# Kernel optimization log

Hardware: AMD Instinct MI355X
Metric: run time of the kernel (lower is better)

The kernel has to match this reference:

```python
import jax, jax.numpy as jnp
import numpy as np

B, S, DIM, N, D = 1, 2688, 1536, 12, 128
C = D // 2  # 64 complex pairs per head
EPS = 1e-06


def rms_norm(x, g, eps=EPS):
    # x: [B, S, DIM] -- norm over full model dim, as in WanRMSNorm
    xf = x.astype(jnp.float32)
    return (xf * jax.lax.rsqrt(jnp.mean(xf * xf, axis=-1, keepdims=True) + eps)) * g


def rope_apply(x, f, h, w, freqs_c):
    # x: [B, S, N, D]; freqs_c: complex64 [1024, C]; f*h*w == S (full-seq case)
    s1 = C - 2 * (C // 3)  # 22 (temporal)
    s2 = C // 3            # 21 (height), 21 (width)
    ff = freqs_c[:f, :s1]
    fh = freqs_c[:h, s1:s1 + s2]
    fw = freqs_c[:w, s1 + s2:]
    fi = jnp.concatenate([
        jnp.broadcast_to(ff[:, None, None, :], (f, h, w, s1)),
        jnp.broadcast_to(fh[None, :, None, :], (f, h, w, s2)),
        jnp.broadcast_to(fw[None, None, :, :], (f, h, w, s2)),
    ], axis=-1).reshape(f * h * w, 1, C)  # [S, 1, C]
    xr = x.astype(jnp.float32).reshape(B, S, N, C, 2)
    xc = jax.lax.complex(xr[..., 0], xr[..., 1])          # [B, S, N, C]
    out = xc * fi[None]                                    # broadcast over B, N
    return jnp.stack([out.real, out.imag], axis=-1).reshape(B, S, N, D)


def setup_inputs() -> dict:
    key = jax.random.key(0)
    ks = jax.random.split(key, 12)
    w_scale = 0.02
    # deterministic rope angles (faithful structure: exp(i*theta) per axis slice)
    pos = np.arange(1024, dtype=np.float32)
    inv = 1.0 / (10000.0 ** (np.arange(C, dtype=np.float32) / C))
    ang = pos[:, None] * inv[None, :]
    return {
        "x": jax.random.normal(ks[0], (B, S, DIM), jnp.float32),
        "seq_lens": jnp.full((B,), S, dtype=jnp.int32),
        "grid_sizes": jnp.array([[6, 16, 28]], dtype=jnp.int32),
        "freqs_cos": jnp.asarray(np.cos(ang), jnp.float32),
        "freqs_sin": jnp.asarray(np.sin(ang), jnp.float32),
        "Wq": jax.random.normal(ks[1], (DIM, DIM), jnp.float32) * w_scale,
        "bq": jnp.zeros((DIM,), jnp.float32),
        "Wk": jax.random.normal(ks[2], (DIM, DIM), jnp.float32) * w_scale,
        "bk": jnp.zeros((DIM,), jnp.float32),
        "Wv": jax.random.normal(ks[3], (DIM, DIM), jnp.float32) * w_scale,
        "bv": jnp.zeros((DIM,), jnp.float32),
        "Wo": jax.random.normal(ks[4], (DIM, DIM), jnp.float32) * w_scale,
        "bo": jnp.zeros((DIM,), jnp.float32),
        "gq": jnp.ones((DIM,), jnp.float32),
        "gk": jnp.ones((DIM,), jnp.float32),
    }


def reference(x, seq_lens, grid_sizes, freqs_cos, freqs_sin,
              Wq, bq, Wk, bk, Wv, bv, Wo, bo, gq, gk):
    f, h, w = (int(grid_sizes[0, 0]), int(grid_sizes[0, 1]), int(grid_sizes[0, 2]))
    freqs_c = jax.lax.complex(freqs_cos, freqs_sin)  # [1024, C]

    q = rms_norm(x @ Wq.T + bq, gq).reshape(B, S, N, D)
    k = rms_norm(x @ Wk.T + bk, gk).reshape(B, S, N, D)
    v = (x @ Wv.T + bv).reshape(B, S, N, D)

    q = rope_apply(q, f, h, w, freqs_c)
    k = rope_apply(k, f, h, w, freqs_c)

    # SDPA with key-length masking (k_lens)
    scale = 1.0 / jnp.sqrt(jnp.float32(D))
    scores = jnp.einsum("bqnd,bknd->bnqk", q, k) * scale  # [B, N, S, S]
    kmask = jnp.arange(S)[None, :] < seq_lens[:, None]     # [B, S]
    scores = jnp.where(kmask[:, None, None, :], scores, -jnp.inf)
    attn = jax.nn.softmax(scores, axis=-1)
    out = jnp.einsum("bnqk,bknd->bqnd", attn, v).reshape(B, S, DIM)
    return out @ Wo.T + bo
```

## Files before the change

### kernel.cpp

```cpp
#include <hip/hip_runtime.h>
#include <hip/hip_bf16.h>
#include <stdint.h>

#define S_LEN 2688
#define DIM   1536
#define NH    12
#define HD    128
#define QKV_N 4608

typedef __attribute__((ext_vector_type(8)))  short bf16x8;
typedef __attribute__((ext_vector_type(4)))  float f32x4;
typedef __attribute__((ext_vector_type(16))) float f32x16;

__device__ inline ushort f2bf(float f) {
    uint32_t u = __float_as_uint(f);
    uint32_t r = (u + 0x7fffu + ((u >> 16) & 1u)) >> 16;
    return (ushort)r;
}
__device__ inline float bf2f(uint u) { return __uint_as_float(u << 16); }
__device__ inline float fexp2(float x) {
    float r;
    asm("v_exp_f32 %0, %1" : "=v"(r) : "v"(x));
    return r;
}
__device__ inline uint cvtpk(float lo, float hi) {
    uint r;
    asm("v_cvt_pk_bf16_f32 %0, %1, %2" : "=v"(r) : "v"(lo), "v"(hi));
    return r;
}

#define GLOAD16(gp, lp) __builtin_amdgcn_global_load_lds( \
    (__attribute__((address_space(1))) const void*)(gp),  \
    (__attribute__((address_space(3))) void*)(lp), 16, 0, 0)

__global__ __launch_bounds__(256) void convert_all(
    const float* __restrict__ x,
    const float* __restrict__ wq, const float* __restrict__ wk,
    const float* __restrict__ wv, const float* __restrict__ wo,
    ushort* __restrict__ xb, ushort* __restrict__ wb)
{
    const size_t NX4 = (size_t)S_LEN * DIM / 4;
    const size_t NW4 = (size_t)DIM * DIM / 4;
    size_t i = (size_t)blockIdx.x * 256 + threadIdx.x;
    const float* src; ushort* dst;
    if (i < NX4)            { src = x;  dst = xb; }
    else if (i < NX4+1*NW4) { src = wq; dst = wb;                        i -= NX4; }
    else if (i < NX4+2*NW4) { src = wk; dst = wb + 1*(size_t)DIM*DIM;    i -= NX4+1*NW4; }
    else if (i < NX4+3*NW4) { src = wv; dst = wb + 2*(size_t)DIM*DIM;    i -= NX4+2*NW4; }
    else if (i < NX4+4*NW4) { src = wo; dst = wb + 3*(size_t)DIM*DIM;    i -= NX4+3*NW4; }
    else return;
    float4 v = reinterpret_cast<const float4*>(src)[i];
    ushort4 o = { f2bf(v.x), f2bf(v.y), f2bf(v.z), f2bf(v.w) };
    reinterpret_cast<ushort4*>(dst)[i] = o;
}

__global__ __launch_bounds__(256) void gemm_qkv(
    const ushort* __restrict__ A, const ushort* __restrict__ B,
    const float* __restrict__ bq, const float* __restrict__ bk,
    const float* __restrict__ bv,
    ushort* __restrict__ qkb, ushort* __restrict__ v_t, int K)
{
    __shared__ ushort At[128 * 64];
    __shared__ ushort Bt[128 * 64];
    const int tid  = threadIdx.x;
    const int wave = tid >> 6, lane = tid & 63;
    const int lid  = blockIdx.y * 21 + blockIdx.x;
    const int xcd  = lid & 7, pos = lid >> 3;
    const int wgid = (xcd < 4 ? xcd * 95 : 4 * 95 + (xcd - 4) * 94) + pos;
    const int m0 = (wgid % 21) * 128, n0 = (wgid / 21) * 128;
    const int wr = wave >> 1, wc = wave & 1;
    const int r = lane & 15, g = lane >> 4;
    const int srow = wave * 8 + (lane >> 3);
    const int scol = (lane & 7) * 8;

    f32x4 acc[4][4] = {};

    for (int k0 = 0; k0 < K; k0 += 64) {
        const ushort* Ag = A + (size_t)m0 * K + k0;
        const ushort* Bg = B + (size_t)n0 * K + k0;
#pragma unroll
        for (int t = 0; t < 4; ++t) {
            GLOAD16(Ag + (size_t)(t*32 + srow) * K + scol, &At[t*2048 + wave*512]);
            GLOAD16(Bg + (size_t)(t*32 + srow) * K + scol, &Bt[t*2048 + wave*512]);
        }
        asm volatile("s_waitcnt vmcnt(0)" ::: "memory");
        __syncthreads();
#pragma unroll
        for (int kk = 0; kk < 2; ++kk) {
            bf16x8 af[4], bfr[4];
#pragma unroll
            for (int i = 0; i < 4; ++i)
                af[i] = *reinterpret_cast<const bf16x8*>(
                    &At[(wr*64 + i*16 + r) * 64 + kk*32 + g*8]);
#pragma unroll
            for (int i = 0; i < 4; ++i)
                bfr[i] = *reinterpret_cast<const bf16x8*>(
                    &Bt[(wc*64 + i*16 + r) * 64 + kk*32 + g*8]);
#pragma unroll
            for (int mi = 0; mi < 4; ++mi)
#pragma unroll
                for (int ni = 0; ni < 4; ++ni)
                    acc[mi][ni] = __builtin_amdgcn_mfma_f32_16x16x32_bf16(
                        af[mi], bfr[ni], acc[mi][ni], 0, 0, 0);
        }
        __syncthreads();
    }

    if (n0 < 2*DIM) {
#pragma unroll
        for (int ni = 0; ni < 4; ++ni) {
            int col = n0 + wc*64 + ni*16 + r;
            float bias = (col < DIM) ? bq[col] : bk[col - DIM];
#pragma unroll
            for (int mi = 0; mi < 4; ++mi) {
                int row = m0 + wr*64 + mi*16 + g*4;
#pragma unroll
                for (int j = 0; j < 4; ++j)
                    qkb[(size_t)(row + j) * (2*DIM) + col] =
                        f2bf(acc[mi][ni][j] + bias);
            }
        }
    } else {
#pragma unroll
        for (int ni = 0; ni < 4; ++ni) {
            int d = n0 - 2*DIM + wc*64 + ni*16 + r;
            float bias = bv[d];
#pragma unroll
            for (int mi = 0; mi < 4; ++mi) {
                int row = m0 + wr*64 + mi*16 + g*4;
                uint2 pkt;
                pkt.x = cvtpk(acc[mi][ni][0] + bias, acc[mi][ni][1] + bias);
                pkt.y = cvtpk(acc[mi][ni][2] + bias, acc[mi][ni][3] + bias);
                *reinterpret_cast<uint2*>(&v_t[(size_t)d * S_LEN + row]) = pkt;
            }
        }
    }
}

__global__ __launch_bounds__(256) void gemm_bt2(
    const ushort* __restrict__ A, const ushort* __restrict__ B,
    const float* __restrict__ b0,
    float* __restrict__ C, int M, int N, int K)
{
    __shared__ ushort At[128 * 64];
    __shared__ ushort Bt[64 * 64];
    const int tid  = threadIdx.x;
    const int wave = tid >> 6, lane = tid & 63;
    const int m0 = blockIdx.x * 128, n0 = blockIdx.y * 64;
    const int wr = wave >> 1, wc = wave & 1;
    const int r = lane & 15, g = lane >> 4;
    const int srow = wave * 8 + (lane >> 3);
    const int scol = (lane & 7) * 8;
    const int brow[2] = { (0*256+tid)>>3, (1*256+tid)>>3 };
    const int bcol = (tid & 7) * 8;

    f32x4 acc[4][2] = {};

    for (int k0 = 0; k0 < K; k0 += 64) {
        const ushort* Ag = A + (size_t)m0 * K + k0;
        const ushort* Bg = B + (size_t)n0 * K + k0;
#pragma unroll
        for (int t = 0; t < 4; ++t)
            GLOAD16(Ag + (size_t)(t*32 + srow) * K + scol, &At[t*2048 + wave*512]);
#pragma unroll
        for (int t = 0; t < 2; ++t)
            GLOAD16(Bg + (size_t)brow[t] * K + bcol, &Bt[(t*256 + wave*64) * 8]);
        asm volatile("s_waitcnt vmcnt(0)" ::: "memory");
        __syncthreads();
#pragma unroll
        for (int kk = 0; kk < 2; ++kk) {
            bf16x8 af[4], bfr[2];
#pragma unroll
            for (int i = 0; i < 4; ++i)
                af[i] = *reinterpret_cast<const bf16x8*>(
                    &At[(wr*64 + i*16 + r) * 64 + kk*32 + g*8]);
#pragma unroll
            for (int i = 0; i < 2; ++i)
                bfr[i] = *reinterpret_cast<const bf16x8*>(
                    &Bt[(wc*32 + i*16 + r) * 64 + kk*32 + g*8]);
#pragma unroll
            for (int mi = 0; mi < 4; ++mi)
#pragma unroll
                for (int ni = 0; ni < 2; ++ni)
                    acc[mi][ni] = __builtin_amdgcn_mfma_f32_16x16x32_bf16(
                        af[mi], bfr[ni], acc[mi][ni], 0, 0, 0);
        }
        __syncthreads();
    }

#pragma unroll
    for (int ni = 0; ni < 2; ++ni) {
        int col = n0 + wc*32 + ni*16 + r;
        float bias = b0[col];
#pragma unroll
        for (int mi = 0; mi < 4; ++mi) {
            int row = m0 + wr*64 + mi*16 + g*4;
#pragma unroll
            for (int j = 0; j < 4; ++j)
                C[(size_t)(row + j) * N + col] = acc[mi][ni][j] + bias;
        }
    }
}

__global__ __launch_bounds__(256) void normrope(
    const ushort* __restrict__ qkb, const int* __restrict__ gsz,
    const float* __restrict__ gq, const float* __restrict__ gk,
    const float* __restrict__ fcos, const float* __restrict__ fsin,
    ushort* __restrict__ q_r, ushort* __restrict__ k_r)
{
    const int s   = blockIdx.x;
    const int tid = threadIdx.x;
    const int wave = tid >> 6, lane = tid & 63;
    const uint* qrow = reinterpret_cast<const uint*>(qkb + (size_t)s * (2*DIM));
    const uint* krow = qrow + DIM/2;

    float2 qv[3], kv[3];
    float sq = 0.f, sk = 0.f;
#pragma unroll
    for (int i = 0; i < 3; ++i) {
        int p = tid + i*256;
        uint uq = qrow[p], uk = krow[p];
        qv[i].x = bf2f(uq & 0xffffu); qv[i].y = bf2f(uq >> 16);
        kv[i].x = bf2f(uk & 0xffffu); kv[i].y = bf2f(uk >> 16);
        sq += qv[i].x*qv[i].x + qv[i].y*qv[i].y;
        sk += kv[i].x*kv[i].x + kv[i].y*kv[i].y;
    }
#pragma unroll
    for (int off = 1; off < 64; off <<= 1) {
        sq += __shfl_xor(sq, off);
        sk += __shfl_xor(sk, off);
    }
    __shared__ float red[4][2];
    if (lane == 0) { red[wave][0] = sq; red[wave][1] = sk; }
    __syncthreads();
    sq = red[0][0] + red[1][0] + red[2][0] + red[3][0];
    sk = red[0][1] + red[1][1] + red[2][1] + red[3][1];
    const float rmsq = rsqrtf(sq * (1.f/DIM) + 1e-6f);
    const float rmsk = rsqrtf(sk * (1.f/DIM) + 1e-6f);

    const int hh = gsz[1], ww = gsz[2];
    const int fidx = s / (hh*ww), rem = s % (hh*ww);
    const int hidx = rem / ww,  widx = rem % ww;
    const float qscale = rmsq * (0.08838834764831845f * 1.4426950408889634f);

#pragma unroll
    for (int i = 0; i < 3; ++i) {
        int p = tid + i*256;
        int c = p & 63, head = p >> 6;
        int coord = (c < 22) ? fidx : (c < 43) ? hidx : widx;
        float cv = fcos[coord*64 + c], sv = fsin[coord*64 + c];
        float2 gqv = reinterpret_cast<const float2*>(gq)[p];
        float2 gkv = reinterpret_cast<const float2*>(gk)[p];
        float a = qv[i].x * qscale * gqv.x, b = qv[i].y * qscale * gqv.y;
        uint qo = cvtpk(a*cv - b*sv, a*sv + b*cv);
        a = kv[i].x * rmsk * gkv.x; b = kv[i].y * rmsk * gkv.y;
        uint ko = cvtpk(a*cv - b*sv, a*sv + b*cv);
        size_t off = (((size_t)head * S_LEN + s) * HD + 2*c) >> 1;
        reinterpret_cast<uint*>(q_r)[off] = qo;
        reinterpret_cast<uint*>(k_r)[off] = ko;
    }
}

__global__ __launch_bounds__(256) void attn_fwd(
    const ushort* __restrict__ q_r, const ushort* __restrict__ k_r,
    const ushort* __restrict__ v_t, const int* __restrict__ seq_lens,
    ushort* __restrict__ attn_out)
{
    __shared__ ushort Kl[2][64 * 128];
    __shared__ ushort Vl[2][128 * 64];
    const int tid  = threadIdx.x;
    const int wave = tid >> 6, lane = tid & 63;
    const int n  = blockIdx.y;
    const int seq = seq_lens[0];
    const int khalf = wave & 1, pair = wave >> 1;
    const int ql = lane & 31, h = lane >> 5, sw = lane & 7;
    const int qrow = blockIdx.x * 64 + pair * 32 + ql;
    const ushort* Qh = q_r + (size_t)n * S_LEN * HD;
    const ushort* Kh = k_r + (size_t)n * S_LEN * HD;
    const ushort* Vh = v_t + (size_t)n * HD * S_LEN;

    const int kj_row[4] = { (0*256+tid)>>4, (1*256+tid)>>4, (2*256+tid)>>4, (3*256+tid)>>4 };
    const int kj_w  = tid & 15;
    const int vj_d[4]  = { (0*256+tid)>>3, (1*256+tid)>>3, (2*256+tid)>>3, (3*256+tid)>>3 };
    const int vj_w  = tid & 7;

    bf16x8 qf[8];
#pragma unroll
    for (int c = 0; c < 8; ++c)
        qf[c] = *reinterpret_cast<const bf16x8*>(Qh + (size_t)qrow * HD + c*16 + h*8);

    f32x16 oacc[4] = {};
    float mrun = -1e30f, lrun = 0.f;

    const int nt = (seq + 63) >> 6;

#define STAGE(buf, kbase)                                                     \
    do {                                                                      \
        _Pragma("unroll")                                                     \
        for (int t = 0; t < 4; ++t) {                                         \
            int row = kj_row[t];                                              \
            GLOAD16(Kh + (size_t)((kbase) + row) * HD + ((kj_w ^ (row & 7)) * 8), \
                    &Kl[buf][(t*256 + wave*64) * 8]);                         \
        }                                                                     \
        _Pragma("unroll")                                                     \
        for (int t = 0; t < 4; ++t) {                                         \
            int d = vj_d[t];                                                  \
            GLOAD16(Vh + (size_t)d * S_LEN + (kbase) + ((vj_w ^ (d & 7)) * 8), \
                    &Vl[buf][(t*256 + wave*64) * 8]);                         \
        }                                                                     \
    } while (0)

    STAGE(0, 0);
    asm volatile("s_waitcnt vmcnt(0)" ::: "memory");
    __syncthreads();

    int cur = 0;
    for (int kt = 0; kt < nt; ++kt) {
        const int k0 = kt * 64 + khalf * 32;
        if (kt + 1 < nt) STAGE(cur ^ 1, (kt+1) * 64);

        f32x16 sf = {};
        const ushort* kl = &Kl[cur][(khalf*32 + ql) * 128];
#pragma unroll
        for (int c = 0; c < 8; ++c)
            sf = __builtin_amdgcn_mfma_f32_32x32x16_bf16(
                *reinterpret_cast<const bf16x8*>(kl + ((2*c + h) ^ sw) * 8),
                qf[c], sf, 0, 0, 0);
        if (k0 + 32 > seq) {
#pragma unroll
            for (int j = 0; j < 16; ++j)
                if (k0 + (j&3) + 8*(j>>2) + 4*h >= seq) sf[j] = -1e30f;
        }
        float pm = sf[0];
#pragma unroll
        for (int j = 1; j < 16; ++j) pm = fmaxf(pm, sf[j]);
        pm = fmaxf(pm, __shfl_xor(pm, 32));
        if (!__all(pm - mrun <= 8.f)) {
            float mn = fmaxf(mrun, pm);
            float scl = fexp2(mrun - mn);
            mrun = mn;
            lrun *= scl;
#pragma unroll
            for (int db = 0; db < 4; ++db)
#pragma unroll
                for (int j = 0; j < 16; ++j) oacc[db][j] *= scl;
        }
        float ps = 0.f;
#pragma unroll
        for (int j = 0; j < 16; ++j) {
            float e = fexp2(sf[j] - mrun);
            sf[j] = e;
            ps += e;
        }
        ps += __shfl_xor(ps, 32);
        lrun += ps;
        uint u0 = cvtpk(sf[0],  sf[1]),  u1 = cvtpk(sf[2],  sf[3]);
        uint u2 = cvtpk(sf[4],  sf[5]),  u3 = cvtpk(sf[6],  sf[7]);
        uint u4 = cvtpk(sf[8],  sf[9]),  u5 = cvtpk(sf[10], sf[11]);
        uint u6 = cvtpk(sf[12], sf[13]), u7 = cvtpk(sf[14], sf[15]);
        asm("v_permlane32_swap_b32 %0, %1" : "+v"(u0), "+v"(u2));
        asm("v_permlane32_swap_b32 %0, %1" : "+v"(u1), "+v"(u3));
        asm("v_permlane32_swap_b32 %0, %1" : "+v"(u4), "+v"(u6));
        asm("v_permlane32_swap_b32 %0, %1" : "+v"(u5), "+v"(u7));
        union { uint uu[4]; bf16x8 v; } fa, fb;
        fa.uu[0] = u0; fa.uu[1] = u1; fa.uu[2] = u2; fa.uu[3] = u3;
        fb.uu[0] = u4; fb.uu[1] = u5; fb.uu[2] = u6; fb.uu[3] = u7;
#pragma unroll
        for (int db = 0; db < 4; ++db) {
            const ushort* vl = &Vl[cur][(db*32 + ql) * 64];
            oacc[db] = __builtin_amdgcn_mfma_f32_32x32x16_bf16(
                *reinterpret_cast<const bf16x8*>(vl + ((khalf*4 + 0 + h) ^ sw) * 8),
                fa.v, oacc[db], 0, 0, 0);
            oacc[db] = __builtin_amdgcn_mfma_f32_32x32x16_bf16(
                *reinterpret_cast<const bf16x8*>(vl + ((khalf*4 + 2 + h) ^ sw) * 8),
                fb.v, oacc[db], 0, 0, 0);
        }

        if (kt + 1 < nt) {
            asm volatile("s_waitcnt vmcnt(0)" ::: "memory");
            __syncthreads();
            cur ^= 1;
        }
    }
#undef STAGE

    __syncthreads();
    float* Obuf  = (float*)&Kl[0][0];
    float* MLbuf = (float*)&Vl[0][0];
    if (khalf == 1) {
#pragma unroll
        for (int db = 0; db < 4; ++db)
#pragma unroll
            for (int j = 0; j < 16; ++j) {
                int d = db*32 + (j&3) + 8*(j>>2) + 4*h;
                Obuf[pair*4096 + d*32 + ql] = oacc[db][j];
            }
        if (h == 0) { MLbuf[pair*64 + ql] = mrun; MLbuf[pair*64 + 32 + ql] = lrun; }
    }
    __syncthreads();
    if (khalf == 0) {
        float m2 = MLbuf[pair*64 + ql], l2 = MLbuf[pair*64 + 32 + ql];
        float mm = fmaxf(mrun, m2);
        float s1 = fexp2(mrun - mm), s2 = fexp2(m2 - mm);
        float ltot = lrun * s1 + l2 * s2;
        float inv = (ltot > 0.f) ? 1.f / ltot : 0.f;
#pragma unroll
        for (int db = 0; db < 4; ++db)
#pragma unroll
            for (int j = 0; j < 16; ++j) {
                int d = db*32 + (j&3) + 8*(j>>2) + 4*h;
                oacc[db][j] = (oacc[db][j] * s1 +
                               Obuf[pair*4096 + d*32 + ql] * s2) * inv;
            }
#pragma unroll
        for (int db = 0; db < 4; ++db)
#pragma unroll
            for (int jg = 0; jg < 4; ++jg) {
                uint2 pkt;
                pkt.x = cvtpk(oacc[db][jg*4+0], oacc[db][jg*4+1]);
                pkt.y = cvtpk(oacc[db][jg*4+2], oacc[db][jg*4+3]);
                *reinterpret_cast<uint2*>(
                    &attn_out[(size_t)qrow * DIM + n*HD + db*32 + jg*8 + 4*h]) = pkt;
            }
    }
}

extern "C" void kernel_launch(void* const* d_in, const int* in_sizes, int n_in,
                              void* d_out, int out_size, void* d_ws, size_t ws_size,
                              hipStream_t stream)
{
    const float* x    = (const float*)d_in[0];
    const int*   seqL = (const int*)  d_in[1];
    const int*   gsz  = (const int*)  d_in[2];
    const float* fcos = (const float*)d_in[3];
    const float* fsin = (const float*)d_in[4];
    const float* Wq   = (const float*)d_in[5];
    const float* bq   = (const float*)d_in[6];
    const float* Wk   = (const float*)d_in[7];
    const float* bk   = (const float*)d_in[8];
    const float* Wv   = (const float*)d_in[9];
    const float* bv   = (const float*)d_in[10];
    const float* Wo   = (const float*)d_in[11];
    const float* bo   = (const float*)d_in[12];
    const float* gq   = (const float*)d_in[13];
    const float* gk   = (const float*)d_in[14];
    float* out = (float*)d_out;

    char* ws = (char*)d_ws;
    ushort* xb  = (ushort*)ws;
    ushort* wb  = xb  + (size_t)S_LEN * DIM;
    ushort* qkb = wb  + 4*(size_t)DIM*DIM;
    ushort* v_t = qkb + (size_t)S_LEN * 2*DIM;
    ushort* q_r = v_t + (size_t)DIM * S_LEN;
    ushort* k_r = q_r + (size_t)S_LEN * DIM;
    ushort* ao  = k_r + (size_t)S_LEN * DIM;

    convert_all<<<13248, 256, 0, stream>>>(x, Wq, Wk, Wv, Wo, xb, wb);
    gemm_qkv<<<dim3(21, 36), 256, 0, stream>>>(xb, wb, bq, bk, bv,
                                               qkb, v_t, DIM);
    normrope<<<S_LEN, 256, 0, stream>>>(qkb, gsz, gq, gk, fcos, fsin, q_r, k_r);
    attn_fwd<<<dim3(42, 12), 256, 0, stream>>>(q_r, k_r, v_t, seqL, ao);
    gemm_bt2<<<dim3(21, 24), 256, 0, stream>>>(ao, wb + 3*(size_t)DIM*DIM,
                                               bo, out, S_LEN, DIM, DIM);
}
```

Baseline: 208.8 us.

## Double-buffer QKV GEMM shared tiles and XOR-swizzle LDS layout

```diff
diff --git a/kernel.cpp b/kernel.cpp
--- a/kernel.cpp
+++ b/kernel.cpp
@@ -60,8 +60,8 @@
     const float* __restrict__ bv,
     ushort* __restrict__ qkb, ushort* __restrict__ v_t, int K)
 {
-    __shared__ ushort At[128 * 64];
-    __shared__ ushort Bt[128 * 64];
+    __shared__ ushort At[2][128 * 64];
+    __shared__ ushort Bt[2][128 * 64];
     const int tid  = threadIdx.x;
     const int wave = tid >> 6, lane = tid & 63;
     const int lid  = blockIdx.y * 21 + blockIdx.x;
@@ -70,32 +70,50 @@
     const int m0 = (wgid % 21) * 128, n0 = (wgid / 21) * 128;
     const int wr = wave >> 1, wc = wave & 1;
     const int r = lane & 15, g = lane >> 4;
-    const int srow = wave * 8 + (lane >> 3);
-    const int scol = (lane & 7) * 8;
+    const int swz = r & 7;
+    const int sj_row[4] = { (0*256+tid)>>3, (1*256+tid)>>3,
+                            (2*256+tid)>>3, (3*256+tid)>>3 };
+    const int sj_w = tid & 7;
 
     f32x4 acc[4][4] = {};
-
-    for (int k0 = 0; k0 < K; k0 += 64) {
-        const ushort* Ag = A + (size_t)m0 * K + k0;
-        const ushort* Bg = B + (size_t)n0 * K + k0;
-#pragma unroll
-        for (int t = 0; t < 4; ++t) {
-            GLOAD16(Ag + (size_t)(t*32 + srow) * K + scol, &At[t*2048 + wave*512]);
-            GLOAD16(Bg + (size_t)(t*32 + srow) * K + scol, &Bt[t*2048 + wave*512]);
-        }
-        asm volatile("s_waitcnt vmcnt(0)" ::: "memory");
-        __syncthreads();
+    const int NT = K >> 6;
+
+#define STAGE_G(buf, kb)                                                      \
+    do {                                                                      \
+        const ushort* Ag = A + (size_t)m0 * K + (kb);                         \
+        const ushort* Bg = B + (size_t)n0 * K + (kb);                         \
+        _Pragma("unroll")                                                     \
+        for (int t = 0; t < 4; ++t) {                                         \
+            int row = sj_row[t];                                              \
+            GLOAD16(Ag + (size_t)row * K + ((sj_w ^ (row & 7)) * 8),          \
+                    &At[buf][(t*256 + tid) * 8]);                             \
+        }                                                                     \
+        _Pragma("unroll")                                                     \
+        for (int t = 0; t < 4; ++t) {                                         \
+            int row = sj_row[t];                                              \
+            GLOAD16(Bg + (size_t)row * K + ((sj_w ^ (row & 7)) * 8),          \
+                    &Bt[buf][(t*256 + tid) * 8]);                             \
+        }                                                                     \
+    } while (0)
+
+    STAGE_G(0, 0);
+    asm volatile("s_waitcnt vmcnt(0)" ::: "memory");
+    __syncthreads();
+
+    int cur = 0;
+    for (int kt = 0; kt < NT; ++kt) {
+        if (kt + 1 < NT) STAGE_G(cur ^ 1, (kt+1) * 64);
 #pragma unroll
         for (int kk = 0; kk < 2; ++kk) {
             bf16x8 af[4], bfr[4];
 #pragma unroll
             for (int i = 0; i < 4; ++i)
                 af[i] = *reinterpret_cast<const bf16x8*>(
-                    &At[(wr*64 + i*16 + r) * 64 + kk*32 + g*8]);
+                    &At[cur][(wr*64 + i*16 + r) * 64 + ((kk*4 + g) ^ swz) * 8]);
 #pragma unroll
             for (int i = 0; i < 4; ++i)
                 bfr[i] = *reinterpret_cast<const bf16x8*>(
-                    &Bt[(wc*64 + i*16 + r) * 64 + kk*32 + g*8]);
+                    &Bt[cur][(wc*64 + i*16 + r) * 64 + ((kk*4 + g) ^ swz) * 8]);
 #pragma unroll
             for (int mi = 0; mi < 4; ++mi)
 #pragma unroll
@@ -103,8 +121,13 @@
                     acc[mi][ni] = __builtin_amdgcn_mfma_f32_16x16x32_bf16(
                         af[mi], bfr[ni], acc[mi][ni], 0, 0, 0);
         }
-        __syncthreads();
-    }
+        if (kt + 1 < NT) {
+            asm volatile("s_waitcnt vmcnt(0)" ::: "memory");
+            __syncthreads();
+            cur ^= 1;
+        }
+    }
+#undef STAGE_G
 
     if (n0 < 2*DIM) {
 #pragma unroll
```

Measured after the change: 192.9 us. 1.08x faster.
